# Kernel tuning notes

Hardware: AMD Instinct MI355X
Metric: run time of the kernel (lower is better)

The kernel has to match this reference:

```python
import jax, jax.numpy as jnp
import numpy as np

GAMMA = 0.5
LENS = 0.5
WINDOW = 10  # window_size from init

@jax.custom_vjp
def act_fun(x):
    # Heaviside forward, Gaussian surrogate backward (matches torch ActFun)
    return (x > 0).astype(x.dtype)

def _act_fwd(x):
    return act_fun(x), x

def _act_bwd(x, g):
    temp = jnp.exp(-x * x / (2 * LENS * LENS)) / (np.sqrt(2 * np.pi) * LENS)
    return (GAMMA * g * temp,)

act_fun.defvjp(_act_fwd, _act_bwd)

def mem_update(inputs, mem, thr):
    # decay_neu == 1
    mem = mem + inputs
    spike = act_fun(mem - thr)
    mem = mem * (1 - spike)
    neg = (mem < -thr).astype(mem.dtype)
    mem = mem * (1 - neg) - thr * neg
    return mem, spike

def setup_inputs() -> dict:
    key = jax.random.key(0)
    ks = jax.random.split(key, 6)
    B, T, D, H, O = 128, 100, 2048, 1024, 20
    return {
        "input": jax.random.normal(ks[0], (B, T, D), jnp.float32),
        "labels": jax.random.randint(ks[1], (B,), 0, O),
        "hidden_mem": jnp.zeros((B, H), jnp.float32),
        "hidden_spike": jnp.zeros((B, H), jnp.float32),
        "output_mem": jnp.zeros((B, O), jnp.float32),
        "output_spike": jnp.zeros((B, O), jnp.float32),
        "Wi2h": jax.random.normal(ks[2], (H, D), jnp.float32) / np.sqrt(D).astype(np.float32),
        "bi2h": jnp.zeros((H,), jnp.float32),
        "Wh2h": jax.random.normal(ks[3], (H, H), jnp.float32) / np.sqrt(H).astype(np.float32),
        "bh2h": jnp.zeros((H,), jnp.float32),
        "Wh2o": jax.random.normal(ks[4], (O, H), jnp.float32) / np.sqrt(H).astype(np.float32),
        "bh2o": jnp.zeros((O,), jnp.float32),
        "thr_h": jnp.ones((H,), jnp.float32),
        "thr_o": jnp.ones((O,), jnp.float32),
    }

def reference(input, labels, hidden_mem, hidden_spike, output_mem, output_spike,
              Wi2h, bi2h, Wh2h, bh2h, Wh2o, bh2o, thr_h, thr_o):
    B = input.shape[0]

    def step(carry, x_t):
        hm, hs, om, osp, osum = carry
        h_in = x_t @ Wi2h.T + bi2h + hs @ Wh2h.T + bh2h
        hm, hs = mem_update(h_in, hm, thr_h)
        om, osp = mem_update(hs @ Wh2o.T + bh2o, om, thr_o)
        osum = osum + osp
        nbr = (jnp.sum(osp) + jnp.sum(hs)) / B
        return (hm, hs, om, osp, osum), (hs, nbr)

    osum0 = jnp.zeros_like(output_spike)
    carry0 = (hidden_mem, hidden_spike, output_mem, output_spike, osum0)
    (hm, hs, om, osp, osum), (hs_t, nbr_events) = jax.lax.scan(
        step, carry0, jnp.swapaxes(input, 0, 1))  # scan over T

    hidden_spike_t = jnp.transpose(hs_t, (1, 2, 0))  # [B, H, T]
    # moving average over time windows (unfold + mean), stride 1
    c = jnp.cumsum(jnp.pad(hidden_spike_t, ((0, 0), (0, 0), (1, 0))), axis=2)
    hidden_spike_filt = (c[:, :, WINDOW:] - c[:, :, :-WINDOW]) / WINDOW  # [B,H,T-W+1]

    logp = jax.nn.log_softmax(osum, axis=1)
    predictions = jnp.argmax(logp, axis=1)[None, :]  # [1, B]
    loss = -jnp.mean(logp[jnp.arange(B), labels])  # NLLLoss on log_softmax
    return predictions, loss, nbr_events, hidden_spike_filt
```

## Files before the change

kernel.cpp:

```cpp
#include <hip/hip_runtime.h>
#include <hip/hip_bf16.h>
#include <cstdint>
#include <cstddef>

#define B_ 128
#define T_ 100
#define D_ 2048
#define H_ 1024
#define O_ 20
#define H2 512

__device__ inline void f4acc(float4& a, const float4 v) {
    a.x += v.x; a.y += v.y; a.z += v.z; a.w += v.w;
}

__global__ __launch_bounds__(256) void prep_kernel(const float* __restrict__ Wh2o,
                                                   float* __restrict__ W2oT,
                                                   float* __restrict__ nbr,
                                                   int* __restrict__ g_flag)
{
    int i = blockIdx.x * 256 + threadIdx.x;
    if (i < H_ * O_) {
        int hh = i / O_;
        int oo = i - hh * O_;
        W2oT[i] = Wh2o[oo * H_ + hh];
    }
    if (i < T_) nbr[i] = 0.0f;
    if (i < B_ * 2) g_flag[i] = 0;
}

__global__ __launch_bounds__(256) void transpose_kernel(const float* __restrict__ A,
                                                        float* __restrict__ AT)
{
    __shared__ float tile[32][33];
    int bx = blockIdx.x * 32, by = blockIdx.y * 32;
    int tx = threadIdx.x, ty = threadIdx.y;
#pragma unroll
    for (int i = 0; i < 32; i += 8)
        tile[ty + i][tx] = A[(size_t)(by + ty + i) * H_ + bx + tx];
    __syncthreads();
#pragma unroll
    for (int i = 0; i < 32; i += 8)
        AT[(size_t)(bx + ty + i) * H_ + by + tx] = tile[tx][ty + i];
}

__global__ __launch_bounds__(256) void gemm_xi_kernel(
    const float* __restrict__ X,
    const float* __restrict__ W,
    const float* __restrict__ bi2h,
    const float* __restrict__ bh2h,
    float* __restrict__ Xi)
{
    constexpr int BM = 128, BN = 128, BK = 16;
    __shared__ float As[BK][BM + 4];
    __shared__ float Bs[BK][BN + 4];
    const int tid = threadIdx.x;
    const int m0 = blockIdx.x * BM;
    const int n0 = blockIdx.y * BN;
    const int wave = tid >> 6;
    const int lane = tid & 63;
    const int tm = ((wave >> 1) << 3) | (lane >> 3);
    const int tn = ((wave & 1) << 3) | (lane & 7);
    const int ldr = tid >> 2;
    const int ldc = (tid & 3) << 2;

    float acc[8][8];
#pragma unroll
    for (int i = 0; i < 8; ++i)
#pragma unroll
        for (int j = 0; j < 8; ++j) acc[i][j] = 0.0f;

    for (int k0 = 0; k0 < D_; k0 += BK) {
#pragma unroll
        for (int p = 0; p < 2; ++p) {
            int r = ldr + p * 64;
            float4 v = *(const float4*)(X + (size_t)(m0 + r) * D_ + k0 + ldc);
            As[ldc + 0][r] = v.x; As[ldc + 1][r] = v.y;
            As[ldc + 2][r] = v.z; As[ldc + 3][r] = v.w;
        }
#pragma unroll
        for (int p = 0; p < 2; ++p) {
            int r = ldr + p * 64;
            float4 v = *(const float4*)(W + (size_t)(n0 + r) * D_ + k0 + ldc);
            Bs[ldc + 0][r] = v.x; Bs[ldc + 1][r] = v.y;
            Bs[ldc + 2][r] = v.z; Bs[ldc + 3][r] = v.w;
        }
        __syncthreads();
#pragma unroll
        for (int k = 0; k < BK; ++k) {
            float4 A0 = *(const float4*)&As[k][tm * 8];
            float4 A1 = *(const float4*)&As[k][tm * 8 + 4];
            float4 B0 = *(const float4*)&Bs[k][tn * 8];
            float4 B1 = *(const float4*)&Bs[k][tn * 8 + 4];
            float a[8] = {A0.x, A0.y, A0.z, A0.w, A1.x, A1.y, A1.z, A1.w};
            float bb[8] = {B0.x, B0.y, B0.z, B0.w, B1.x, B1.y, B1.z, B1.w};
#pragma unroll
            for (int i = 0; i < 8; ++i)
#pragma unroll
                for (int j = 0; j < 8; ++j) acc[i][j] += a[i] * bb[j];
        }
        __syncthreads();
    }

    float bsum[8];
#pragma unroll
    for (int j = 0; j < 8; ++j) {
        int n = n0 + tn * 8 + j;
        bsum[j] = bi2h[n] + bh2h[n];
    }
#pragma unroll
    for (int i = 0; i < 8; ++i) {
        size_t row = (size_t)(m0 + tm * 8 + i);
        float4 o0 = {acc[i][0] + bsum[0], acc[i][1] + bsum[1],
                     acc[i][2] + bsum[2], acc[i][3] + bsum[3]};
        float4 o1 = {acc[i][4] + bsum[4], acc[i][5] + bsum[5],
                     acc[i][6] + bsum[6], acc[i][7] + bsum[7]};
        *(float4*)(Xi + row * H_ + n0 + tn * 8)     = o0;
        *(float4*)(Xi + row * H_ + n0 + tn * 8 + 4) = o1;
    }
}

__global__ __launch_bounds__(512) void phase2_kernel(
    const float* __restrict__ Xi,
    const float* __restrict__ WT,
    const float* __restrict__ W2oT,
    const float* __restrict__ bh2o,
    const float* __restrict__ thr_h_g,
    const float* __restrict__ thr_o_g,
    const float* __restrict__ hm0,
    const float* __restrict__ hs0,
    const float* __restrict__ om0,
    unsigned long long* __restrict__ g_mask,
    float* __restrict__ g_opart,
    int* __restrict__ g_flag,
    ulonglong2* __restrict__ spk,
    float* __restrict__ osum_out,
    float* __restrict__ nbr_acc)
{
    const int pair = blockIdx.x >> 1;
    const int half = blockIdx.x & 1;
    const int b = pair;
    const int tid = threadIdx.x;
    const int lane = tid & 63;
    const int wv = tid >> 6;
    const int h0 = half * H2;
    const int h = h0 + tid;

    __shared__ float s_W2o[H2 * O_];
    __shared__ int   s_list[H_];
    __shared__ float4 s_red[4][128];
    __shared__ unsigned long long s_mask[16];
    __shared__ float s_opart[8][O_];
    __shared__ float s_popart[O_];
    __shared__ int   s_base[16];
    __shared__ int   s_cnt;
    __shared__ float s_om[O_], s_osum[O_], s_tho[O_], s_bo[O_];

    for (int idx = tid; idx < H2 * O_; idx += 512)
        s_W2o[idx] = W2oT[h0 * O_ + idx];

    float hm = hm0[(size_t)b * H_ + h];
    const float thr = thr_h_g[h];

    if (half == 0 && tid < O_) {
        s_om[tid]   = om0[b * O_ + tid];
        s_osum[tid] = 0.0f;
        s_tho[tid]  = thr_o_g[tid];
        s_bo[tid]   = bh2o[tid];
    }

    {
        bool a1 = hs0[(size_t)b * H_ + wv * 64 + lane] > 0.5f;
        bool a2 = hs0[(size_t)b * H_ + H2 + wv * 64 + lane] > 0.5f;
        unsigned long long m1 = __ballot(a1), m2 = __ballot(a2);
        if (lane == 0) { s_mask[wv] = m1; s_mask[8 + wv] = m2; }
    }
    __syncthreads();
    if (tid == 0) {
        int a = 0;
#pragma unroll
        for (int w = 0; w < 16; ++w) { s_base[w] = a; a += __popcll(s_mask[w]); }
        s_cnt = a;
    }
    __syncthreads();
    {
        int j = tid; int w = j >> 6; unsigned long long mw = s_mask[w];
        if ((mw >> (j & 63)) & 1ull)
            s_list[s_base[w] + __popcll(mw & ((1ull << (j & 63)) - 1ull))] = j;
        j = tid + H2; w = j >> 6; mw = s_mask[w];
        if ((mw >> (j & 63)) & 1ull)
            s_list[s_base[w] + __popcll(mw & ((1ull << (j & 63)) - 1ull))] = j;
    }
    __syncthreads();

    const float4* __restrict__ wt4 = (const float4*)WT + (h0 >> 2);
    const int g = tid >> 7;
    const int cid = tid & 127;
    unsigned long long bits0 = 0, bits1 = 0;

    for (int t = 0; t < T_; ++t) {
        const int cnt = s_cnt;
        float4 a0 = {0,0,0,0}, a1 = {0,0,0,0}, a2 = {0,0,0,0}, a3 = {0,0,0,0};
        int l = g;
        for (; l + 12 < cnt; l += 16) {
            int j0 = s_list[l], j1 = s_list[l + 4], j2 = s_list[l + 8], j3 = s_list[l + 12];
            f4acc(a0, wt4[(size_t)j0 * 256 + cid]);
            f4acc(a1, wt4[(size_t)j1 * 256 + cid]);
            f4acc(a2, wt4[(size_t)j2 * 256 + cid]);
            f4acc(a3, wt4[(size_t)j3 * 256 + cid]);
        }
        for (; l < cnt; l += 4) f4acc(a0, wt4[(size_t)s_list[l] * 256 + cid]);
        f4acc(a0, a1); f4acc(a2, a3); f4acc(a0, a2);
        s_red[g][cid] = a0;
        __syncthreads();

        float val = 0.0f;
        const float* rf = (const float*)s_red;
#pragma unroll
        for (int gg = 0; gg < 4; ++gg) val += rf[gg * 512 + tid];

        hm += Xi[((size_t)b * T_ + t) * H_ + h] + val;
        bool sp = (hm - thr) > 0.0f;
        if (sp) hm = 0.0f;
        if (hm < -thr) hm = -thr;
        if (sp) { if (t < 64) bits0 |= (1ull << t); else bits1 |= (1ull << (t - 64)); }

        unsigned long long m = __ballot(sp);
        const int myword = half * 8 + wv;
        if (lane == 0) s_mask[myword] = m;

        float op = 0.0f;
        if (lane < O_) {
            unsigned long long mm = m;
            while (mm) {
                int bit = __builtin_ctzll(mm);
                mm &= mm - 1;
                op += s_W2o[(wv * 64 + bit) * O_ + lane];
            }
            s_opart[wv][lane] = op;
        }

        const int buf = t & 1;
        unsigned long long* gm = g_mask + (((size_t)(pair * 2 + buf) * 2 + half) * 8);
        if (lane == 0)
            __hip_atomic_store(&gm[wv], m, __ATOMIC_RELAXED, __HIP_MEMORY_SCOPE_AGENT);
        __syncthreads();

        float ownpart = 0.0f;
        if (tid < O_) {
            float s = 0.0f;
#pragma unroll
            for (int w = 0; w < 8; ++w) s += s_opart[w][tid];
            ownpart = s;
            float* go = g_opart + (((size_t)(pair * 2 + buf) * 2 + half) * O_);
            __hip_atomic_store(&go[tid], s, __ATOMIC_RELAXED, __HIP_MEMORY_SCOPE_AGENT);
        }
        __syncthreads();
        if (tid == 0) {
            __hip_atomic_store(&g_flag[pair * 2 + half], t + 1,
                               __ATOMIC_RELEASE, __HIP_MEMORY_SCOPE_AGENT);
            while (__hip_atomic_load(&g_flag[pair * 2 + (half ^ 1)],
                                     __ATOMIC_ACQUIRE, __HIP_MEMORY_SCOPE_AGENT) < t + 1)
                __builtin_amdgcn_s_sleep(1);
        }
        __syncthreads();

        const unsigned long long* pm =
            g_mask + (((size_t)(pair * 2 + buf) * 2 + (half ^ 1)) * 8);
        if (tid < 8)
            s_mask[(half ^ 1) * 8 + tid] =
                __hip_atomic_load(&pm[tid], __ATOMIC_RELAXED, __HIP_MEMORY_SCOPE_AGENT);
        if (half == 0 && tid < O_) {
            const float* po = g_opart + (((size_t)(pair * 2 + buf) * 2 + 1) * O_);
            s_popart[tid] =
                __hip_atomic_load(&po[tid], __ATOMIC_RELAXED, __HIP_MEMORY_SCOPE_AGENT);
        }
        __syncthreads();

        if (half == 0) {
            float osp_l = 0.0f;
            if (tid < O_) {
                float oin = s_bo[tid] + ownpart + s_popart[tid];
                float om = s_om[tid] + oin;
                float osp = ((om - s_tho[tid]) > 0.0f) ? 1.0f : 0.0f;
                if (osp > 0.5f) om = 0.0f;
                if (om < -s_tho[tid]) om = -s_tho[tid];
                s_om[tid] = om;
                s_osum[tid] += osp;
                osp_l = osp;
            }
            if (wv == 0) {
                float c = osp_l;
                c += __shfl_xor(c, 1);  c += __shfl_xor(c, 2);
                c += __shfl_xor(c, 4);  c += __shfl_xor(c, 8);
                c += __shfl_xor(c, 16); c += __shfl_xor(c, 32);
                if (lane == 0) {
                    int hc = 0;
#pragma unroll
                    for (int w = 0; w < 16; ++w) hc += __popcll(s_mask[w]);
                    atomicAdd(&nbr_acc[t], c + (float)hc);
                }
            }
        }

        if (tid == 0) {
            int a = 0;
#pragma unroll
            for (int w = 0; w < 16; ++w) { s_base[w] = a; a += __popcll(s_mask[w]); }
            s_cnt = a;
        }
        __syncthreads();
        {
            int j = tid; int w = j >> 6; unsigned long long mw = s_mask[w];
            if ((mw >> (j & 63)) & 1ull)
                s_list[s_base[w] + __popcll(mw & ((1ull << (j & 63)) - 1ull))] = j;
            j = tid + H2; w = j >> 6; mw = s_mask[w];
            if ((mw >> (j & 63)) & 1ull)
                s_list[s_base[w] + __popcll(mw & ((1ull << (j & 63)) - 1ull))] = j;
        }
        __syncthreads();
    }

    ulonglong2 vv; vv.x = bits0; vv.y = bits1;
    spk[(size_t)b * H_ + h] = vv;
    if (half == 0 && tid < O_) osum_out[b * O_ + tid] = s_osum[tid];
}

__global__ __launch_bounds__(256) void filt_kernel(const ulonglong2* __restrict__ spk,
                                                   float* __restrict__ outf)
{
    int i = blockIdx.x * 256 + threadIdx.x;
    ulonglong2 v = spk[i];
    float* o = outf + (size_t)i * 91;
    int s = __popcll(v.x & 0x3FFull);
    o[0] = (float)s * 0.1f;
#pragma unroll 1
    for (int tau = 1; tau <= 90; ++tau) {
        int ta = tau + 9, tsb = tau - 1;
        int add = (ta < 64) ? (int)((v.x >> ta) & 1ull) : (int)((v.y >> (ta - 64)) & 1ull);
        int sub = (tsb < 64) ? (int)((v.x >> tsb) & 1ull) : (int)((v.y >> (tsb - 64)) & 1ull);
        s += add - sub;
        o[tau] = (float)s * 0.1f;
    }
}

__global__ __launch_bounds__(256) void final_kernel(const float* __restrict__ osum,
                                                    const int* __restrict__ labels,
                                                    float* __restrict__ dout)
{
    __shared__ float s_loss[B_];
    int tid = threadIdx.x;
    if (tid < B_) {
        int b = tid;
        float v[O_];
#pragma unroll
        for (int o = 0; o < O_; ++o) v[o] = osum[b * O_ + o];
        float mv = v[0];
        int am = 0;
#pragma unroll
        for (int o = 1; o < O_; ++o)
            if (v[o] > mv) { mv = v[o]; am = o; }
        float se = 0.0f;
#pragma unroll
        for (int o = 0; o < O_; ++o) se += expf(v[o] - mv);
        float lse = mv + logf(se);
        dout[b] = (float)am;
        s_loss[b] = v[labels[b]] - lse;
    }
    if (tid >= 128 && tid < 128 + T_) {
        dout[129 + (tid - 128)] *= (1.0f / (float)B_);
    }
    __syncthreads();
    if (tid == 0) {
        float s = 0.0f;
        for (int b = 0; b < B_; ++b) s += s_loss[b];
        dout[128] = -s / (float)B_;
    }
}

extern "C" void kernel_launch(void* const* d_in, const int* in_sizes, int n_in,
                              void* d_out, int out_size, void* d_ws, size_t ws_size,
                              hipStream_t stream)
{
    const float* input  = (const float*)d_in[0];
    const int*   labels = (const int*)d_in[1];
    const float* hm0    = (const float*)d_in[2];
    const float* hs0    = (const float*)d_in[3];
    const float* om0    = (const float*)d_in[4];
    const float* Wi2h   = (const float*)d_in[6];
    const float* bi2h   = (const float*)d_in[7];
    const float* Wh2h   = (const float*)d_in[8];
    const float* bh2h   = (const float*)d_in[9];
    const float* Wh2o   = (const float*)d_in[10];
    const float* bh2o   = (const float*)d_in[11];
    const float* thr_h  = (const float*)d_in[12];
    const float* thr_o  = (const float*)d_in[13];

    float* out  = (float*)d_out;
    float* nbr  = out + 129;
    float* filt = out + 229;

    char* ws = (char*)d_ws;
    float*      Xi     = (float*)(ws);
    float*      WT     = (float*)(ws + 52428800);
    float*      W2oT   = (float*)(ws + 56623104);
    ulonglong2* spk    = (ulonglong2*)(ws + 56705024);
    float*      osum   = (float*)(ws + 58802176);
    unsigned long long* g_mask = (unsigned long long*)(ws + 58812416);
    float*      g_opart = (float*)(ws + 58845184);
    int*        g_flag  = (int*)(ws + 58886144);

    prep_kernel<<<80, 256, 0, stream>>>(Wh2o, W2oT, nbr, g_flag);
    transpose_kernel<<<dim3(32, 32), dim3(32, 8), 0, stream>>>(Wh2h, WT);
    gemm_xi_kernel<<<dim3(100, 8), 256, 0, stream>>>(input, Wi2h, bi2h, bh2h, Xi);
    phase2_kernel<<<256, 512, 0, stream>>>(Xi, WT, W2oT, bh2o, thr_h, thr_o,
                                           hm0, hs0, om0, g_mask, g_opart, g_flag,
                                           spk, osum, nbr);
    filt_kernel<<<512, 256, 0, stream>>>(spk, filt);
    final_kernel<<<1, 256, 0, stream>>>(osum, labels, out);
}
```

Before: 2.057 ms.

## Overlap own-half spike gather with partner handshake and defer output layer

The recurrent step now splits the sparse weight gather into two parts. The block accumulates rows for its own spikes before it waits on the partner block's flag, then does the partner's rows after the handshake. The output-layer update is moved one step later and done only by the half-0 block, which reads the global W2oT through both spike lists, so the per-step exchange of partial output sums and one barrier round are gone. Block index mapping changes so the two halves of a batch row are 128 blocks apart, and the gather is unrolled to 8 accumulators. The gain depends on hiding synchronization latency; the costs are an extra loop iteration and uncached global reads of W2oT.

```diff
diff --git a/kernel.cpp b/kernel.cpp
--- a/kernel.cpp
+++ b/kernel.cpp
@@ -131,33 +131,26 @@
     const float* __restrict__ hs0,
     const float* __restrict__ om0,
     unsigned long long* __restrict__ g_mask,
-    float* __restrict__ g_opart,
     int* __restrict__ g_flag,
     ulonglong2* __restrict__ spk,
     float* __restrict__ osum_out,
     float* __restrict__ nbr_acc)
 {
-    const int pair = blockIdx.x >> 1;
-    const int half = blockIdx.x & 1;
+    const int pair = blockIdx.x & 127;
+    const int half = blockIdx.x >> 7;
     const int b = pair;
     const int tid = threadIdx.x;
     const int lane = tid & 63;
     const int wv = tid >> 6;
     const int h0 = half * H2;
+    const int ph0 = h0 ^ H2;
     const int h = h0 + tid;
 
-    __shared__ float s_W2o[H2 * O_];
-    __shared__ int   s_list[H_];
+    __shared__ int   s_list[1024];
     __shared__ float4 s_red[4][128];
     __shared__ unsigned long long s_mask[16];
     __shared__ float s_opart[8][O_];
-    __shared__ float s_popart[O_];
-    __shared__ int   s_base[16];
-    __shared__ int   s_cnt;
     __shared__ float s_om[O_], s_osum[O_], s_tho[O_], s_bo[O_];
-
-    for (int idx = tid; idx < H2 * O_; idx += 512)
-        s_W2o[idx] = W2oT[h0 * O_ + idx];
 
     float hm = hm0[(size_t)b * H_ + h];
     const float thr = thr_h_g[h];
@@ -170,117 +163,154 @@
     }
 
     {
-        bool a1 = hs0[(size_t)b * H_ + wv * 64 + lane] > 0.5f;
-        bool a2 = hs0[(size_t)b * H_ + H2 + wv * 64 + lane] > 0.5f;
-        unsigned long long m1 = __ballot(a1), m2 = __ballot(a2);
-        if (lane == 0) { s_mask[wv] = m1; s_mask[8 + wv] = m2; }
+        bool own = hs0[(size_t)b * H_ + h] > 0.5f;
+        bool par = hs0[(size_t)b * H_ + ph0 + tid] > 0.5f;
+        unsigned long long mo = __ballot(own), mp = __ballot(par);
+        if (lane == 0) { s_mask[half * 8 + wv] = mo; s_mask[(half ^ 1) * 8 + wv] = mp; }
     }
     __syncthreads();
-    if (tid == 0) {
-        int a = 0;
-#pragma unroll
-        for (int w = 0; w < 16; ++w) { s_base[w] = a; a += __popcll(s_mask[w]); }
-        s_cnt = a;
+
+    int cnt_own;
+    {
+        const int ow = half * 8;
+        int pc[8];
+#pragma unroll
+        for (int k = 0; k < 8; ++k) pc[k] = __popcll(s_mask[ow + k]);
+        int basew = 0, tot = 0;
+#pragma unroll
+        for (int k = 0; k < 8; ++k) { if (k < wv) basew += pc[k]; tot += pc[k]; }
+        cnt_own = tot;
+        unsigned long long mw = s_mask[ow + wv];
+        if ((mw >> lane) & 1ull)
+            s_list[basew + __popcll(mw & ((1ull << lane) - 1ull))] = h;
     }
     __syncthreads();
-    {
-        int j = tid; int w = j >> 6; unsigned long long mw = s_mask[w];
-        if ((mw >> (j & 63)) & 1ull)
-            s_list[s_base[w] + __popcll(mw & ((1ull << (j & 63)) - 1ull))] = j;
-        j = tid + H2; w = j >> 6; mw = s_mask[w];
-        if ((mw >> (j & 63)) & 1ull)
-            s_list[s_base[w] + __popcll(mw & ((1ull << (j & 63)) - 1ull))] = j;
-    }
-    __syncthreads();
-
-    const float4* __restrict__ wt4 = (const float4*)WT + (h0 >> 2);
+
+    const float4* __restrict__ wt4b = (const float4*)WT + (h0 >> 2);
     const int g = tid >> 7;
     const int cid = tid & 127;
+    const int fl_partner = pair * 2 + (half ^ 1);
+    const int fl_self    = pair * 2 + half;
     unsigned long long bits0 = 0, bits1 = 0;
 
-    for (int t = 0; t < T_; ++t) {
-        const int cnt = s_cnt;
-        float4 a0 = {0,0,0,0}, a1 = {0,0,0,0}, a2 = {0,0,0,0}, a3 = {0,0,0,0};
-        int l = g;
-        for (; l + 12 < cnt; l += 16) {
-            int j0 = s_list[l], j1 = s_list[l + 4], j2 = s_list[l + 8], j3 = s_list[l + 12];
-            f4acc(a0, wt4[(size_t)j0 * 256 + cid]);
-            f4acc(a1, wt4[(size_t)j1 * 256 + cid]);
-            f4acc(a2, wt4[(size_t)j2 * 256 + cid]);
-            f4acc(a3, wt4[(size_t)j3 * 256 + cid]);
-        }
-        for (; l < cnt; l += 4) f4acc(a0, wt4[(size_t)s_list[l] * 256 + cid]);
-        f4acc(a0, a1); f4acc(a2, a3); f4acc(a0, a2);
-        s_red[g][cid] = a0;
-        __syncthreads();
-
-        float val = 0.0f;
-        const float* rf = (const float*)s_red;
-#pragma unroll
-        for (int gg = 0; gg < 4; ++gg) val += rf[gg * 512 + tid];
-
-        hm += Xi[((size_t)b * T_ + t) * H_ + h] + val;
-        bool sp = (hm - thr) > 0.0f;
-        if (sp) hm = 0.0f;
-        if (hm < -thr) hm = -thr;
-        if (sp) { if (t < 64) bits0 |= (1ull << t); else bits1 |= (1ull << (t - 64)); }
-
-        unsigned long long m = __ballot(sp);
-        const int myword = half * 8 + wv;
-        if (lane == 0) s_mask[myword] = m;
-
-        float op = 0.0f;
-        if (lane < O_) {
-            unsigned long long mm = m;
-            while (mm) {
-                int bit = __builtin_ctzll(mm);
-                mm &= mm - 1;
-                op += s_W2o[(wv * 64 + bit) * O_ + lane];
+    for (int t = 0; t <= T_; ++t) {
+        const bool full = (t < T_);
+        float xi = 0.0f;
+        if (full) xi = Xi[((size_t)b * T_ + t) * H_ + h];
+
+        float4 c0 = {0,0,0,0}, c1 = {0,0,0,0}, c2 = {0,0,0,0}, c3 = {0,0,0,0};
+        float4 c4 = {0,0,0,0}, c5 = {0,0,0,0}, c6 = {0,0,0,0}, c7 = {0,0,0,0};
+
+        if (full) {
+            const int c = cnt_own;
+            int l = g;
+            for (; l + 28 < c; l += 32) {
+                int j0 = s_list[l],      j1 = s_list[l + 4];
+                int j2 = s_list[l + 8],  j3 = s_list[l + 12];
+                int j4 = s_list[l + 16], j5 = s_list[l + 20];
+                int j6 = s_list[l + 24], j7 = s_list[l + 28];
+                f4acc(c0, wt4b[(size_t)j0 * 256 + cid]);
+                f4acc(c1, wt4b[(size_t)j1 * 256 + cid]);
+                f4acc(c2, wt4b[(size_t)j2 * 256 + cid]);
+                f4acc(c3, wt4b[(size_t)j3 * 256 + cid]);
+                f4acc(c4, wt4b[(size_t)j4 * 256 + cid]);
+                f4acc(c5, wt4b[(size_t)j5 * 256 + cid]);
+                f4acc(c6, wt4b[(size_t)j6 * 256 + cid]);
+                f4acc(c7, wt4b[(size_t)j7 * 256 + cid]);
             }
-            s_opart[wv][lane] = op;
-        }
-
-        const int buf = t & 1;
-        unsigned long long* gm = g_mask + (((size_t)(pair * 2 + buf) * 2 + half) * 8);
-        if (lane == 0)
-            __hip_atomic_store(&gm[wv], m, __ATOMIC_RELAXED, __HIP_MEMORY_SCOPE_AGENT);
-        __syncthreads();
-
-        float ownpart = 0.0f;
-        if (tid < O_) {
-            float s = 0.0f;
-#pragma unroll
-            for (int w = 0; w < 8; ++w) s += s_opart[w][tid];
-            ownpart = s;
-            float* go = g_opart + (((size_t)(pair * 2 + buf) * 2 + half) * O_);
-            __hip_atomic_store(&go[tid], s, __ATOMIC_RELAXED, __HIP_MEMORY_SCOPE_AGENT);
-        }
-        __syncthreads();
-        if (tid == 0) {
-            __hip_atomic_store(&g_flag[pair * 2 + half], t + 1,
-                               __ATOMIC_RELEASE, __HIP_MEMORY_SCOPE_AGENT);
-            while (__hip_atomic_load(&g_flag[pair * 2 + (half ^ 1)],
-                                     __ATOMIC_ACQUIRE, __HIP_MEMORY_SCOPE_AGENT) < t + 1)
+            for (; l < c; l += 4) f4acc(c0, wt4b[(size_t)s_list[l] * 256 + cid]);
+        }
+
+        if (t > 0 && tid == 0) {
+            while (__hip_atomic_load(&g_flag[fl_partner], __ATOMIC_ACQUIRE,
+                                     __HIP_MEMORY_SCOPE_AGENT) < t)
                 __builtin_amdgcn_s_sleep(1);
         }
         __syncthreads();
-
-        const unsigned long long* pm =
-            g_mask + (((size_t)(pair * 2 + buf) * 2 + (half ^ 1)) * 8);
-        if (tid < 8)
+        if (t > 0 && tid < 8) {
+            const unsigned long long* pm =
+                g_mask + (((size_t)(pair * 2 + ((t - 1) & 1)) * 2 + (half ^ 1)) * 8);
             s_mask[(half ^ 1) * 8 + tid] =
                 __hip_atomic_load(&pm[tid], __ATOMIC_RELAXED, __HIP_MEMORY_SCOPE_AGENT);
-        if (half == 0 && tid < O_) {
-            const float* po = g_opart + (((size_t)(pair * 2 + buf) * 2 + 1) * O_);
-            s_popart[tid] =
-                __hip_atomic_load(&po[tid], __ATOMIC_RELAXED, __HIP_MEMORY_SCOPE_AGENT);
-        }
-        __syncthreads();
-
-        if (half == 0) {
+        }
+        __syncthreads();
+
+        int cnt_p;
+        {
+            const int pw = (half ^ 1) * 8;
+            int pc[8];
+#pragma unroll
+            for (int k = 0; k < 8; ++k) pc[k] = __popcll(s_mask[pw + k]);
+            int basew = 0, tot = 0;
+#pragma unroll
+            for (int k = 0; k < 8; ++k) { if (k < wv) basew += pc[k]; tot += pc[k]; }
+            cnt_p = tot;
+            unsigned long long mw = s_mask[pw + wv];
+            if ((mw >> lane) & 1ull)
+                s_list[512 + basew + __popcll(mw & ((1ull << lane) - 1ull))] =
+                    ph0 + wv * 64 + lane;
+        }
+        __syncthreads();
+
+        if (full) {
+            const int c = cnt_p;
+            int l = g;
+            for (; l + 28 < c; l += 32) {
+                int j0 = s_list[512 + l],      j1 = s_list[512 + l + 4];
+                int j2 = s_list[512 + l + 8],  j3 = s_list[512 + l + 12];
+                int j4 = s_list[512 + l + 16], j5 = s_list[512 + l + 20];
+                int j6 = s_list[512 + l + 24], j7 = s_list[512 + l + 28];
+                f4acc(c0, wt4b[(size_t)j0 * 256 + cid]);
+                f4acc(c1, wt4b[(size_t)j1 * 256 + cid]);
+                f4acc(c2, wt4b[(size_t)j2 * 256 + cid]);
+                f4acc(c3, wt4b[(size_t)j3 * 256 + cid]);
+                f4acc(c4, wt4b[(size_t)j4 * 256 + cid]);
+                f4acc(c5, wt4b[(size_t)j5 * 256 + cid]);
+                f4acc(c6, wt4b[(size_t)j6 * 256 + cid]);
+                f4acc(c7, wt4b[(size_t)j7 * 256 + cid]);
+            }
+            for (; l < c; l += 4) f4acc(c0, wt4b[(size_t)s_list[512 + l] * 256 + cid]);
+        }
+
+        if (half == 0 && t > 0 && lane < O_) {
+            float op = 0.0f;
+            for (int q = wv; q < cnt_own; q += 8) op += W2oT[s_list[q] * O_ + lane];
+            for (int q = wv; q < cnt_p; q += 8)  op += W2oT[s_list[512 + q] * O_ + lane];
+            s_opart[wv][lane] = op;
+        }
+
+        {
+            f4acc(c0, c1); f4acc(c2, c3); f4acc(c4, c5); f4acc(c6, c7);
+            f4acc(c0, c2); f4acc(c4, c6); f4acc(c0, c4);
+            s_red[g][cid] = c0;
+        }
+        const int hidprev = cnt_own + cnt_p;
+        __syncthreads();
+
+        if (full) {
+            const float* rf = (const float*)s_red;
+            float val = rf[tid] + rf[512 + tid] + rf[1024 + tid] + rf[1536 + tid];
+            hm += xi + val;
+            bool sp = (hm - thr) > 0.0f;
+            if (sp) hm = 0.0f;
+            if (hm < -thr) hm = -thr;
+            if (sp) { if (t < 64) bits0 |= 1ull << t; else bits1 |= 1ull << (t - 64); }
+            unsigned long long m = __ballot(sp);
+            if (lane == 0) {
+                s_mask[half * 8 + wv] = m;
+                unsigned long long* gm =
+                    g_mask + (((size_t)(pair * 2 + (t & 1)) * 2 + half) * 8);
+                __hip_atomic_store(&gm[wv], m, __ATOMIC_RELAXED,
+                                   __HIP_MEMORY_SCOPE_AGENT);
+            }
+        }
+
+        if (half == 0 && t > 0) {
             float osp_l = 0.0f;
             if (tid < O_) {
-                float oin = s_bo[tid] + ownpart + s_popart[tid];
+                float oin = s_bo[tid];
+#pragma unroll
+                for (int w = 0; w < 8; ++w) oin += s_opart[w][tid];
                 float om = s_om[tid] + oin;
                 float osp = ((om - s_tho[tid]) > 0.0f) ? 1.0f : 0.0f;
                 if (osp > 0.5f) om = 0.0f;
@@ -290,33 +320,30 @@
                 osp_l = osp;
             }
             if (wv == 0) {
-                float c = osp_l;
-                c += __shfl_xor(c, 1);  c += __shfl_xor(c, 2);
-                c += __shfl_xor(c, 4);  c += __shfl_xor(c, 8);
-                c += __shfl_xor(c, 16); c += __shfl_xor(c, 32);
-                if (lane == 0) {
-                    int hc = 0;
-#pragma unroll
-                    for (int w = 0; w < 16; ++w) hc += __popcll(s_mask[w]);
-                    atomicAdd(&nbr_acc[t], c + (float)hc);
-                }
+                float cc = osp_l;
+                cc += __shfl_xor(cc, 1);  cc += __shfl_xor(cc, 2);
+                cc += __shfl_xor(cc, 4);  cc += __shfl_xor(cc, 8);
+                cc += __shfl_xor(cc, 16); cc += __shfl_xor(cc, 32);
+                if (lane == 0)
+                    atomicAdd(&nbr_acc[t - 1], cc + (float)hidprev);
             }
         }
-
-        if (tid == 0) {
-            int a = 0;
-#pragma unroll
-            for (int w = 0; w < 16; ++w) { s_base[w] = a; a += __popcll(s_mask[w]); }
-            s_cnt = a;
-        }
-        __syncthreads();
-        {
-            int j = tid; int w = j >> 6; unsigned long long mw = s_mask[w];
-            if ((mw >> (j & 63)) & 1ull)
-                s_list[s_base[w] + __popcll(mw & ((1ull << (j & 63)) - 1ull))] = j;
-            j = tid + H2; w = j >> 6; mw = s_mask[w];
-            if ((mw >> (j & 63)) & 1ull)
-                s_list[s_base[w] + __popcll(mw & ((1ull << (j & 63)) - 1ull))] = j;
+        __syncthreads();
+        if (full && tid == 0)
+            __hip_atomic_store(&g_flag[fl_self], t + 1, __ATOMIC_RELEASE,
+                               __HIP_MEMORY_SCOPE_AGENT);
+        if (full) {
+            const int ow = half * 8;
+            int pc[8];
+#pragma unroll
+            for (int k = 0; k < 8; ++k) pc[k] = __popcll(s_mask[ow + k]);
+            int basew = 0, tot = 0;
+#pragma unroll
+            for (int k = 0; k < 8; ++k) { if (k < wv) basew += pc[k]; tot += pc[k]; }
+            cnt_own = tot;
+            unsigned long long mw = s_mask[ow + wv];
+            if ((mw >> lane) & 1ull)
+                s_list[basew + __popcll(mw & ((1ull << lane) - 1ull))] = h;
         }
         __syncthreads();
     }
@@ -407,14 +434,13 @@
     ulonglong2* spk    = (ulonglong2*)(ws + 56705024);
     float*      osum   = (float*)(ws + 58802176);
     unsigned long long* g_mask = (unsigned long long*)(ws + 58812416);
-    float*      g_opart = (float*)(ws + 58845184);
-    int*        g_flag  = (int*)(ws + 58886144);
+    int*        g_flag  = (int*)(ws + 58845184);
 
     prep_kernel<<<80, 256, 0, stream>>>(Wh2o, W2oT, nbr, g_flag);
     transpose_kernel<<<dim3(32, 32), dim3(32, 8), 0, stream>>>(Wh2h, WT);
     gemm_xi_kernel<<<dim3(100, 8), 256, 0, stream>>>(input, Wi2h, bi2h, bh2h, Xi);
     phase2_kernel<<<256, 512, 0, stream>>>(Xi, WT, W2oT, bh2o, thr_h, thr_o,
-                                           hm0, hs0, om0, g_mask, g_opart, g_flag,
+                                           hm0, hs0, om0, g_mask, g_flag,
                                            spk, osum, nbr);
     filt_kernel<<<512, 256, 0, stream>>>(spk, filt);
     final_kernel<<<1, 256, 0, stream>>>(osum, labels, out);
```

Result: slower. 3.202 ms (+55.7%).
